# Optimization experiments

Hardware: AMD Instinct MI355X
Metric: run time of the kernel (lower is better)

The kernel has to match this reference:

```python
import jax, jax.numpy as jnp
import numpy as np

# Hardware-emulation constants (from init_kwargs, NeuroSim-style QLinear)
WL_IN = 8        # input activation bit width (bit-serial)
WL_W = 8         # weight bit width
CELL_BIT = 2     # bits per memory cell -> 4 weight slices
SUB = 128        # crossbar sub-array size (rows summed in analog)
ADC_BITS = 5     # ADC precision per partial sum
ONOFF = 10.0     # cell on/off conductance ratio
VARI = 0.05      # multiplicative device variation sigma


def _adc_quant(x, bits, axes):
    # LinearQuantizeOut: uniform quantization between tensor min/max
    mn = jnp.min(x, axis=axes, keepdims=True)
    mx = jnp.max(x, axis=axes, keepdims=True)
    step = (mx - mn) * (2.0 ** (-bits))
    step = jnp.where(step <= 0, 1.0, step)
    idx = jnp.clip(jnp.floor((x - mn) / step), 0.0, 2.0 ** bits - 1.0)
    return idx * step + mn


def _qlinear_hw(x, w, noise):
    """Analog PIM crossbar emulation of y = x @ w.T with bit-serial inputs,
    bit-sliced cells, on/off-ratio offset + dummy column, device variation,
    per-subarray ADC quantization."""
    B, N = x.shape
    F = w.shape[0]
    I, W, K = WL_IN, WL_W, WL_W // CELL_BIT
    cr = 2.0 ** CELL_BIT
    lower, upper = 1.0 / ONOFF, 1.0
    S = (N + SUB - 1) // SUB
    Np = S * SUB
    # quantize input to I bits in [0,1]; weight to W-bit integer in [0, 2^W-1]
    xq = jnp.round(jnp.clip(x, 0.0, 1.0) * (2.0 ** I - 1.0))            # [B, N]
    Xi = jnp.clip(jnp.round((w + 1.0) * 0.5 * (2.0 ** W - 1.0)), 0.0, 2.0 ** W - 1.0)  # [F, N]
    xq = jnp.pad(xq, ((0, 0), (0, Np - N)))
    Xi = jnp.pad(Xi, ((0, 0), (0, Np - N)))
    zpow = 2.0 ** jnp.arange(I, dtype=x.dtype)
    kpow = cr ** jnp.arange(K, dtype=x.dtype)
    bits = jnp.mod(jnp.floor(xq[..., None] / zpow), 2.0)                # [B, Np, I]
    slc = jnp.mod(jnp.floor(Xi[..., None] / kpow), cr)                  # [F, Np, K]
    g = slc * (upper - lower) + (cr - 1.0) * lower                      # cell conductances
    g = g * (1.0 + VARI * noise)                                        # device variation
    bits = bits.reshape(B, S, SUB, I)
    g = g.reshape(F, S, SUB, K)
    # analog partial sums per (input bit i, subarray s, weight slice k)
    P = jnp.einsum('bsai,fsak->iskbf', bits, g)                         # [I,S,K,B,F]
    # dummy column (all cells at lowest conductance), identical across F
    D = jnp.transpose(bits.sum(axis=2), (2, 1, 0)) * ((cr - 1.0) * lower)  # [I,S,B]
    Pq = _adc_quant(P, ADC_BITS, axes=(3, 4))
    Dq = _adc_quant(D, ADC_BITS, axes=(2,))
    scal = (2.0 ** jnp.arange(I, dtype=x.dtype))[:, None] * (cr ** jnp.arange(K, dtype=x.dtype))[None, :]
    acc = jnp.einsum('iskbf,ik->bf', Pq - Dq[:, :, None, :, None], scal) / (upper - lower)
    # undo integer mappings: w = 2*Xi/(2^W-1) - 1, x = xq/(2^I-1)
    out = 2.0 * acc / ((2.0 ** I - 1.0) * (2.0 ** W - 1.0)) \
          - xq.sum(axis=1, keepdims=True) / (2.0 ** I - 1.0)
    return out


def _qlinear(x, w, noise):
    # straight-through quantized weight (WAGE-style STE) + hardware forward
    Xi = jnp.clip(jnp.round((w + 1.0) * 0.5 * (2.0 ** WL_W - 1.0)), 0.0, 2.0 ** WL_W - 1.0)
    wq = 2.0 * Xi / (2.0 ** WL_W - 1.0) - 1.0
    wq_ste = w + jax.lax.stop_gradient(wq - w)
    out_ideal = x @ wq_ste.T
    out_hw = _qlinear_hw(x, w, noise)
    return out_ideal + jax.lax.stop_gradient(out_hw - out_ideal)


def setup_inputs() -> dict:
    key = jax.random.key(0)
    k1, k2, k3, k4, k5 = jax.random.split(key, 5)
    x = jax.random.uniform(k1, (1024, 784), dtype=jnp.float32)
    w1 = jax.random.normal(k2, (512, 784), dtype=jnp.float32) * 0.05
    w3 = jax.random.normal(k3, (10, 512), dtype=jnp.float32) * 0.08
    noise1 = jax.random.normal(k4, (512, 896, 4), dtype=jnp.float32)  # 784 padded to 7*128
    noise3 = jax.random.normal(k5, (10, 512, 4), dtype=jnp.float32)   # 512 = 4*128 exact
    return {"x": x, "w1": w1, "w3": w3, "noise1": noise1, "noise3": noise3}


def reference(x, w1, w3, noise1, noise3):
    h = jnp.tanh(_qlinear(x, w1, noise1))   # QLinear(784,512) + Tanh
    return _qlinear(h, w3, noise3)          # QLinear(512,10)
```

## Files before the change

### kernel.cpp

```cpp
#include <hip/hip_runtime.h>

#define FLTMAX 3.402823466e+38f


__device__ __forceinline__ void grid_barrier(unsigned* bar, int s, unsigned nblk)
{
    __syncthreads();
    if (threadIdx.x == 0) {
        unsigned* ctr = bar + s * 128;
        unsigned* rel = bar + 896 + s * 16;
        asm volatile("s_waitcnt vmcnt(0)" ::: "memory");
        __hip_atomic_fetch_add(&ctr[(blockIdx.x & 7) << 4], 1u,
                               __ATOMIC_RELAXED, __HIP_MEMORY_SCOPE_AGENT);
        if (blockIdx.x == 0) {
            for (int it = 0; it < (1 << 20); ++it) {
                unsigned tot = 0;
#pragma unroll
                for (int j = 0; j < 8; ++j)
                    tot += __hip_atomic_load(&ctr[j << 4], __ATOMIC_RELAXED,
                                             __HIP_MEMORY_SCOPE_AGENT);
                if (tot >= nblk) break;
                __builtin_amdgcn_s_sleep(8);
            }
            __hip_atomic_store(rel, 1u, __ATOMIC_RELAXED, __HIP_MEMORY_SCOPE_AGENT);
        } else {
            for (int it = 0; it < (1 << 20); ++it) {
                if (__hip_atomic_load(rel, __ATOMIC_RELAXED,
                                      __HIP_MEMORY_SCOPE_AGENT) != 0u)
                    break;
                __builtin_amdgcn_s_sleep(16);
            }
        }
    }
    __syncthreads();
}

__global__ void prep1_kernel(const float* __restrict__ x, float* __restrict__ sx1,
                             unsigned* __restrict__ xqbT, unsigned* __restrict__ stats1,
                             unsigned* __restrict__ bar)
{
    __shared__ float xr[896];
    __shared__ float red[128];
    int b = blockIdx.x;
    if (b == 0) {
        for (int t = threadIdx.x; t < 224; t += 128) {
            stats1[t * 2] = 0x7F7FFFFFu; stats1[t * 2 + 1] = 0u;
        }
        for (int t = threadIdx.x; t < 1008; t += 128) bar[t] = 0u;
    }
    float psum = 0.f;
    for (int n = threadIdx.x; n < 896; n += 128) {
        float v = 0.f;
        if (n < 784) {
            float xv = x[b * 784 + n];
            xv = fminf(fmaxf(xv, 0.f), 1.f);
            v = rintf(__fmul_rn(xv, 255.f));
        }
        xr[n] = v;
        psum += v;
    }
    red[threadIdx.x] = psum;
    __syncthreads();
    for (int w = 64; w >= 1; w >>= 1) {
        if (threadIdx.x < w) red[threadIdx.x] += red[threadIdx.x + w];
        __syncthreads();
    }
    if (threadIdx.x == 0) sx1[b] = red[0];
    if (threadIdx.x < 28) {
        int w = threadIdx.x;
        unsigned words[8] = {0, 0, 0, 0, 0, 0, 0, 0};
#pragma unroll 8
        for (int n = 0; n < 32; ++n) {
            int v = (int)xr[w * 32 + n];
#pragma unroll
            for (int i = 0; i < 8; ++i) words[i] |= ((unsigned)((v >> i) & 1)) << n;
        }
#pragma unroll
        for (int i = 0; i < 8; ++i) xqbT[(i * 28 + w) * 1024 + b] = words[i];
    }
}

__global__ void prepg1t_kernel(const float* __restrict__ w1, const float* __restrict__ noise1,
                               float* __restrict__ g1t)
{
    __shared__ float t[4][32][33];
    const int n0 = blockIdx.x * 32, f0 = blockIdx.y * 32;
    const int tid = threadIdx.x;
    {
        int n = tid & 31, fi = tid >> 5;
#pragma unroll
        for (int p = 0; p < 4; ++p) {
            int f = p * 8 + fi;
            int gn = n0 + n, gf = f0 + f;
            float gv[4] = {0.f, 0.f, 0.f, 0.f};
            if (gn < 784) {
                float w = w1[gf * 784 + gn];
                float Xi = fminf(fmaxf(rintf(__fmul_rn(__fmul_rn(__fadd_rn(w, 1.f), 0.5f), 255.f)),
                                       0.f), 255.f);
                int xi = (int)Xi;
                float4 nz = *(const float4*)&noise1[(gf * 896 + gn) * 4];
                float nzv[4] = {nz.x, nz.y, nz.z, nz.w};
#pragma unroll
                for (int k = 0; k < 4; ++k) {
                    int slc = (xi >> (2 * k)) & 3;
                    float base = __fadd_rn(__fmul_rn((float)slc, 0.9f), 0.3f);
                    float nf = __fadd_rn(1.f, __fmul_rn(0.05f, nzv[k]));
                    gv[k] = __fmul_rn(base, nf);
                }
            }
#pragma unroll
            for (int k = 0; k < 4; ++k) t[k][n][f] = gv[k];
        }
    }
    __syncthreads();
    {
        int f = tid & 31, nn = tid >> 5;
#pragma unroll
        for (int p = 0; p < 4; ++p) {
            int n = p * 8 + nn;
#pragma unroll
            for (int k = 0; k < 4; ++k)
                g1t[(n0 + n) * 2048 + k * 512 + f0 + f] = t[k][n][f];
        }
    }
}

__global__ void prepg2_kernel(const float* __restrict__ w3, const float* __restrict__ noise3,
                              float* __restrict__ g2t)
{
    int gid = blockIdx.x * 256 + threadIdx.x;
    if (gid >= 10 * 512) return;
    int f = gid / 512, n = gid % 512;
    float w = w3[f * 512 + n];
    float Xi = fminf(fmaxf(rintf(__fmul_rn(__fmul_rn(__fadd_rn(w, 1.f), 0.5f), 255.f)),
                           0.f), 255.f);
    int xi = (int)Xi;
#pragma unroll
    for (int k = 0; k < 4; ++k) {
        int slc = (xi >> (2 * k)) & 3;
        float base = __fadd_rn(__fmul_rn((float)slc, 0.9f), 0.3f);
        float nf = __fadd_rn(1.f, __fmul_rn(0.05f, noise3[(f * 512 + n) * 4 + k]));
        g2t[n * 40 + k * 10 + f] = __fmul_rn(base, nf);
    }
}

__global__ void dqpopT_kernel(const unsigned* __restrict__ xqbT, float* __restrict__ Dq)
{
    __shared__ float red[512];
    const int i = blockIdx.x / 7, s = blockIdx.x % 7;
    const int tid = threadIdx.x;
    float D[4];
    float mn = FLTMAX, mx = -FLTMAX;
#pragma unroll
    for (int u = 0; u < 4; ++u) {
        int b = tid + u * 256;
        int c = 0;
#pragma unroll
        for (int w = 0; w < 4; ++w)
            c += __popc(xqbT[(i * 28 + s * 4 + w) * 1024 + b]);
        D[u] = __fmul_rn((float)c, 0.3f);
        mn = fminf(mn, D[u]);
        mx = fmaxf(mx, D[u]);
    }
    red[tid] = mn; red[256 + tid] = mx;
    __syncthreads();
    for (int w = 128; w >= 1; w >>= 1) {
        if (tid < w) {
            red[tid] = fminf(red[tid], red[tid + w]);
            red[256 + tid] = fmaxf(red[256 + tid], red[256 + tid + w]);
        }
        __syncthreads();
    }
    mn = red[0]; mx = red[256];
    float step = __fmul_rn(__fsub_rn(mx, mn), 0.03125f);
    if (step <= 0.f) step = 1.f;
#pragma unroll
    for (int u = 0; u < 4; ++u) {
        int b = tid + u * 256;
        float idx = fminf(fmaxf(floorf(__fdiv_rn(__fsub_rn(D[u], mn), step)), 0.f), 31.f);
        Dq[(i * 7 + s) * 1024 + b] = __fadd_rn(__fmul_rn(idx, step), mn);
    }
}

__global__ void dqpop_kernel(const unsigned* __restrict__ xqb, float* __restrict__ Dq,
                             int S, int wpr)
{
    __shared__ float red[512];
    const int i = blockIdx.x / S, s = blockIdx.x % S;
    const int tid = threadIdx.x;
    float D[4];
    float mn = FLTMAX, mx = -FLTMAX;
#pragma unroll
    for (int u = 0; u < 4; ++u) {
        int b = tid + u * 256;
        uint4 w = *(const uint4*)&xqb[(i * 1024 + b) * wpr + s * 4];
        int c = __popc(w.x) + __popc(w.y) + __popc(w.z) + __popc(w.w);
        D[u] = __fmul_rn((float)c, 0.3f);
        mn = fminf(mn, D[u]);
        mx = fmaxf(mx, D[u]);
    }
    red[tid] = mn; red[256 + tid] = mx;
    __syncthreads();
    for (int w = 128; w >= 1; w >>= 1) {
        if (tid < w) {
            red[tid] = fminf(red[tid], red[tid + w]);
            red[256 + tid] = fmaxf(red[256 + tid], red[256 + tid + w]);
        }
        __syncthreads();
    }
    mn = red[0]; mx = red[256];
    float step = __fmul_rn(__fsub_rn(mx, mn), 0.03125f);
    if (step <= 0.f) step = 1.f;
#pragma unroll
    for (int u = 0; u < 4; ++u) {
        int b = tid + u * 256;
        float idx = fminf(fmaxf(floorf(__fdiv_rn(__fsub_rn(D[u], mn), step)), 0.f), 31.f);
        Dq[(i * S + s) * 1024 + b] = __fadd_rn(__fmul_rn(idx, step), mn);
    }
}

#define BK 32
__global__ __launch_bounds__(256, 2) void mm1_kernel(
    const unsigned* __restrict__ xqbT, const float* __restrict__ g1t,
    unsigned char* __restrict__ Pidx, unsigned* stats, unsigned* bar)
{
    __shared__ __align__(16) float Bs[BK][132];
    __shared__ unsigned Abits[256];
    __shared__ float red[512];
    __shared__ __align__(16) unsigned stage[2][128 * 33];
    const int tid = threadIdx.x;
    const int pair = blockIdx.x & 31;
    const int i = pair >> 2;
    const int bp = (pair & 3) * 256;
    const int btile0 = (pair * 2) & 7;
    const int colgrp = blockIdx.x >> 5;
    const int colBase = colgrp * 128;
    const int tx = tid & 15, ty = tid >> 4;
    const int aB = tid >> 5;
    const int eB = (tid & 31) << 2;
    const int k = colgrp >> 2;
    const int wv = tid >> 6, ln = tid & 63;
    const int rsub = ln >> 3, chunk = ln & 7;

    for (int s = 0; s < 7; ++s) {
        float4 pB[4];
#pragma unroll
        for (int u = 0; u < 4; ++u)
            pB[u] = *(const float4*)&g1t[(s * 128 + u * 8 + aB) * 2048 + colBase + eB];
        unsigned pAw = xqbT[(i * 28 + s * 4) * 1024 + bp + tid];

        float acc[2][8][8] = {};

        for (int ac = 0; ac < 4; ++ac) {
            __syncthreads();
#pragma unroll
            for (int u = 0; u < 4; ++u)
                *(float4*)&Bs[u * 8 + aB][eB] = pB[u];
            Abits[tid] = pAw;
            __syncthreads();

            if (ac < 3) {
                const int n0 = s * 128 + (ac + 1) * BK;
#pragma unroll
                for (int u = 0; u < 4; ++u)
                    pB[u] = *(const float4*)&g1t[(n0 + u * 8 + aB) * 2048 + colBase + eB];
                pAw = xqbT[(i * 28 + s * 4 + ac + 1) * 1024 + bp + tid];
            }

            unsigned wrd[2][8];
#pragma unroll
            for (int q = 0; q < 2; ++q)
#pragma unroll
                for (int u = 0; u < 4; ++u) {
                    wrd[q][u]     = Abits[q * 128 + (ty << 2) + u];
                    wrd[q][4 + u] = Abits[q * 128 + 64 + (ty << 2) + u];
                }

#pragma unroll 4
            for (int a = 0; a < BK; ++a) {
                float br[8];
                *(float4*)&br[0] = *(const float4*)&Bs[a][(tx << 2)];
                *(float4*)&br[4] = *(const float4*)&Bs[a][64 + (tx << 2)];
#pragma unroll
                for (int q = 0; q < 2; ++q)
#pragma unroll
                    for (int u = 0; u < 8; ++u) {
                        float ab = (float)((wrd[q][u] >> a) & 1u);
#pragma unroll
                        for (int v = 0; v < 8; ++v)
                            acc[q][u][v] = fmaf(ab, br[v], acc[q][u][v]);
                    }
            }
        }

        float mn = acc[0][0][0], mx = acc[0][0][0];
#pragma unroll
        for (int q = 0; q < 2; ++q)
#pragma unroll
            for (int u = 0; u < 8; ++u)
#pragma unroll
                for (int v = 0; v < 8; ++v) {
                    mn = fminf(mn, acc[q][u][v]); mx = fmaxf(mx, acc[q][u][v]);
                }
        red[tid] = mn; red[256 + tid] = mx;
        __syncthreads();
        for (int w = 128; w >= 1; w >>= 1) {
            if (tid < w) {
                red[tid] = fminf(red[tid], red[tid + w]);
                red[256 + tid] = fmaxf(red[256 + tid], red[256 + tid + w]);
            }
            __syncthreads();
        }
        const int slot = ((s * 8 + i) * 4 + k) * 2;
        if (tid == 0) {
            atomicMin(&stats[slot], __float_as_uint(red[0]));
            atomicMax(&stats[slot + 1], __float_as_uint(red[256]));
        }

        grid_barrier(bar, s, 512u);

        unsigned mnu = __hip_atomic_load(&stats[slot],     __ATOMIC_RELAXED,
                                         __HIP_MEMORY_SCOPE_AGENT);
        unsigned mxu = __hip_atomic_load(&stats[slot + 1], __ATOMIC_RELAXED,
                                         __HIP_MEMORY_SCOPE_AGENT);
        float qmn = __uint_as_float(mnu);
        float qmx = __uint_as_float(mxu);
        float step = __fmul_rn(__fsub_rn(qmx, qmn), 0.03125f);
        if (step <= 0.f) step = 1.f;

#pragma unroll
        for (int q = 0; q < 2; ++q)
#pragma unroll
            for (int uh = 0; uh < 2; ++uh)
#pragma unroll
                for (int u = 0; u < 4; ++u) {
                    int rr = uh * 64 + (ty << 2) + u;
#pragma unroll
                    for (int vh = 0; vh < 2; ++vh) {
                        float ix;
                        unsigned pack;
                        ix = fminf(fmaxf(floorf(__fdiv_rn(__fsub_rn(acc[q][uh * 4 + u][vh * 4 + 0], qmn), step)), 0.f), 31.f);
                        pack = (unsigned)(int)ix;
                        ix = fminf(fmaxf(floorf(__fdiv_rn(__fsub_rn(acc[q][uh * 4 + u][vh * 4 + 1], qmn), step)), 0.f), 31.f);
                        pack |= (unsigned)(int)ix << 8;
                        ix = fminf(fmaxf(floorf(__fdiv_rn(__fsub_rn(acc[q][uh * 4 + u][vh * 4 + 2], qmn), step)), 0.f), 31.f);
                        pack |= (unsigned)(int)ix << 16;
                        ix = fminf(fmaxf(floorf(__fdiv_rn(__fsub_rn(acc[q][uh * 4 + u][vh * 4 + 3], qmn), step)), 0.f), 31.f);
                        pack |= (unsigned)(int)ix << 24;
                        stage[q][rr * 33 + vh * 16 + tx] = pack;
                    }
                }
        __syncthreads();

#pragma unroll
        for (int q = 0; q < 2; ++q) {
            unsigned char* tbase = Pidx +
                ((size_t)(((s * 8 + i) * 16 + colgrp) * 8 + btile0 + q)) * 16384;
#pragma unroll
            for (int t = 0; t < 4; ++t) {
                int rr = t * 32 + wv * 8 + rsub;
                const unsigned* sp = &stage[q][rr * 33 + chunk * 4];
                uint4 v = make_uint4(sp[0], sp[1], sp[2], sp[3]);
                *(uint4*)&tbase[rr * 128 + chunk * 16] = v;
            }
        }
    }
}

__global__ void fold1_kernel(const unsigned char* __restrict__ Pidx,
                             const unsigned* __restrict__ stats,
                             const float* __restrict__ Dq1, const float* __restrict__ sx1,
                             float* __restrict__ xq2, unsigned* __restrict__ xqb2,
                             float* __restrict__ sx2)
{
    __shared__ float red[512];
    __shared__ float dt;
    __shared__ float2 st[224];
    int b = blockIdx.x;
    int f = threadIdx.x;
    if (f < 224) {
        float mn = __uint_as_float(stats[f * 2]);
        float mx = __uint_as_float(stats[f * 2 + 1]);
        float step = __fmul_rn(__fsub_rn(mx, mn), 0.03125f);
        if (step <= 0.f) step = 1.f;
        st[f] = make_float2(mn, step);
    }
    if (f == 0) {
        float sd = 0.f;
        for (int i = 0; i < 8; ++i) {
            float sc = (float)(85 << i);
            for (int ss = 0; ss < 7; ++ss) sd = fmaf(Dq1[(i * 7 + ss) * 1024 + b], sc, sd);
        }
        dt = sd;
    }
    __syncthreads();
    const int fhi = f >> 7, fl = f & 127;
    const unsigned char* pb = Pidx + (size_t)(b >> 7) * 16384
                                   + (size_t)(b & 127) * 128 + fl;
    float accR = 0.f;
    for (int s = 0; s < 7; ++s) {
        float sum = 0.f;
        for (int i = 0; i < 8; ++i) {
            const int si16 = (s * 8 + i) * 16;
#pragma unroll
            for (int kk = 0; kk < 4; ++kk) {
                float2 ms = st[((s * 8 + i) << 2) + kk];
                float ixv = (float)pb[(size_t)(si16 + kk * 4 + fhi) * 131072];
                float pq = __fadd_rn(__fmul_rn(ixv, ms.y), ms.x);
                sum = fmaf(pq, (float)(1 << (i + 2 * kk)), sum);
            }
        }
        accR = __fadd_rn(accR, sum);
    }
    float total = __fsub_rn(accR, dt);
    float acc = __fdiv_rn(total, 0.9f);
    float o = __fsub_rn(__fdiv_rn(__fmul_rn(2.f, acc), 65025.f), __fdiv_rn(sx1[b], 255.f));
    float h = tanhf(o);
    h = fminf(fmaxf(h, 0.f), 1.f);
    float code = rintf(__fmul_rn(h, 255.f));
    xq2[b * 512 + f] = code;
    int ci = (int)code;
    int lane = f & 63;
#pragma unroll
    for (int i = 0; i < 8; ++i) {
        unsigned long long m = __ballot((ci >> i) & 1);
        if ((lane & 31) == 0) {
            unsigned wv = (lane & 32) ? (unsigned)(m >> 32) : (unsigned)m;
            xqb2[(i * 1024 + b) * 16 + (f >> 5)] = wv;
        }
    }
    red[f] = code;
    __syncthreads();
    for (int w = 256; w >= 1; w >>= 1) {
        if (f < w) red[f] += red[f + w];
        __syncthreads();
    }
    if (f == 0) sx2[b] = red[0];
}

__global__ void mm2_kernel(const float* __restrict__ xq2, const float* __restrict__ g2t,
                           float* __restrict__ P2)
{
    int gid = blockIdx.x * 256 + threadIdx.x;
    if (gid >= 40960) return;
    int f = gid % 10;
    int b = (gid / 10) & 1023;
    int s = gid / 10240;
    float acc[8][4] = {};
    for (int a = 0; a < 128; ++a) {
        int n = s * 128 + a;
        int xi = (int)xq2[b * 512 + n];
        float g0 = g2t[n * 40 + f];
        float gA = g2t[n * 40 + 10 + f];
        float gB = g2t[n * 40 + 20 + f];
        float gC = g2t[n * 40 + 30 + f];
#pragma unroll
        for (int i = 0; i < 8; ++i) {
            float bi = (float)((xi >> i) & 1);
            acc[i][0] = fmaf(bi, g0, acc[i][0]);
            acc[i][1] = fmaf(bi, gA, acc[i][1]);
            acc[i][2] = fmaf(bi, gB, acc[i][2]);
            acc[i][3] = fmaf(bi, gC, acc[i][3]);
        }
    }
#pragma unroll
    for (int i = 0; i < 8; ++i)
#pragma unroll
        for (int k = 0; k < 4; ++k)
            P2[(size_t)((s * 8 + i) * 4 + k) * 10240 + b * 10 + f] = acc[i][k];
}

__global__ void stat2_kernel(const float* __restrict__ P2, float2* __restrict__ stats2)
{
    __shared__ float red[512];
    int p = blockIdx.x;
    int tid = threadIdx.x;
    float mn = FLTMAX, mx = -FLTMAX;
    for (int t = tid; t < 10240; t += 256) {
        float v = P2[(size_t)p * 10240 + t];
        mn = fminf(mn, v); mx = fmaxf(mx, v);
    }
    red[tid] = mn; red[256 + tid] = mx;
    __syncthreads();
    for (int w = 128; w >= 1; w >>= 1) {
        if (tid < w) {
            red[tid] = fminf(red[tid], red[tid + w]);
            red[256 + tid] = fmaxf(red[256 + tid], red[256 + tid + w]);
        }
        __syncthreads();
    }
    if (tid == 0) {
        float step = __fmul_rn(__fsub_rn(red[256], red[0]), 0.03125f);
        if (step <= 0.f) step = 1.f;
        stats2[p] = make_float2(red[0], step);
    }
}

__global__ void out2_kernel(const float* __restrict__ P2, const float2* __restrict__ stats2,
                            const float* __restrict__ Dq2, const float* __restrict__ sx2,
                            float* __restrict__ out)
{
    int gid = blockIdx.x * 256 + threadIdx.x;
    if (gid >= 10240) return;
    int b = gid / 10;
    float dt = 0.f;
    for (int i = 0; i < 8; ++i) {
        float sc = (float)(85 << i);
        for (int s = 0; s < 4; ++s) dt = fmaf(Dq2[(i * 4 + s) * 1024 + b], sc, dt);
    }
    float sum = 0.f;
    for (int s = 0; s < 4; ++s)
        for (int i = 0; i < 8; ++i)
#pragma unroll
            for (int k = 0; k < 4; ++k) {
                int p = (s * 8 + i) * 4 + k;
                float2 st = stats2[p];
                float val = P2[(size_t)p * 10240 + gid];
                float idx = fminf(fmaxf(floorf(__fdiv_rn(__fsub_rn(val, st.x), st.y)), 0.f), 31.f);
                float pq = __fadd_rn(__fmul_rn(idx, st.y), st.x);
                sum = fmaf(pq, (float)(1 << (i + 2 * k)), sum);
            }
    float total = __fsub_rn(sum, dt);
    float acc = __fdiv_rn(total, 0.9f);
    out[gid] = __fsub_rn(__fdiv_rn(__fmul_rn(2.f, acc), 65025.f), __fdiv_rn(sx2[b], 255.f));
}

extern "C" void kernel_launch(void* const* d_in, const int* in_sizes, int n_in,
                              void* d_out, int out_size, void* d_ws, size_t ws_size,
                              hipStream_t stream)
{
    const float* x      = (const float*)d_in[0];
    const float* w1     = (const float*)d_in[1];
    const float* w3     = (const float*)d_in[2];
    const float* noise1 = (const float*)d_in[3];
    const float* noise3 = (const float*)d_in[4];
    float* out = (float*)d_out;
    float* ws  = (float*)d_ws;

    float*         g1t    = ws + 0;
    float*         xq2    = ws + 1835008;
    float*         P2     = ws + 2359296;
    float*         g2t    = ws + 3670016;
    float*         Dq1    = ws + 3690496;
    float*         Dq2    = ws + 3747840;
    float*         sx1    = ws + 3780608;
    float*         sx2    = ws + 3781632;
    float2*        stats2 = (float2*)(ws + 3782656);
    unsigned*      stats1 = (unsigned*)(ws + 3782912);
    unsigned*      xqbT   = (unsigned*)(ws + 3783424);
    unsigned*      xqb2   = (unsigned*)(ws + 4012800);
    unsigned char* Pidx   = (unsigned char*)(ws + 4143872);
    unsigned*      bar    = (unsigned*)(ws + 33504256);

    prep1_kernel<<<1024, 128, 0, stream>>>(x, sx1, xqbT, stats1, bar);
    prepg1t_kernel<<<dim3(28, 16), 256, 0, stream>>>(w1, noise1, g1t);
    dqpopT_kernel<<<56, 256, 0, stream>>>(xqbT, Dq1);

    mm1_kernel<<<512, 256, 0, stream>>>(xqbT, g1t, Pidx, stats1, bar);

    fold1_kernel<<<1024, 512, 0, stream>>>(Pidx, stats1, Dq1, sx1, xq2, xqb2, sx2);
    prepg2_kernel<<<20, 256, 0, stream>>>(w3, noise3, g2t);
    dqpop_kernel<<<32, 256, 0, stream>>>(xqb2, Dq2, 4, 16);
    mm2_kernel<<<160, 256, 0, stream>>>(xq2, g2t, P2);
    stat2_kernel<<<128, 256, 0, stream>>>(P2, stats2);
    out2_kernel<<<40, 256, 0, stream>>>(P2, stats2, Dq2, sx2, out);
}
```

Baseline: 634.2 us.

## Replace grid-wide barrier with per-slot barriers and use packed FMA

Each persistent block used to wait at a grid-wide barrier after every subarray step. It now waits only on a per-statistics-slot counter that the 16 blocks sharing that ADC min/max slot increment, which removes global serialization across all 512 blocks. The inner accumulation is also rewritten with 2-wide float vectors so the compiler can emit packed FMA (v_pk_fma_f32) instructions. A trailing __syncthreads is added to protect the staging buffer, and the barrier memory cleared at startup grows to fit the per-slot counters.

```diff
diff --git a/kernel.cpp b/kernel.cpp
--- a/kernel.cpp
+++ b/kernel.cpp
@@ -2,34 +2,19 @@
 
 #define FLTMAX 3.402823466e+38f
 
-
-__device__ __forceinline__ void grid_barrier(unsigned* bar, int s, unsigned nblk)
+typedef float f32x2 __attribute__((ext_vector_type(2)));
+
+
+__device__ __forceinline__ void slot_barrier(unsigned* ctr, unsigned target)
 {
     __syncthreads();
     if (threadIdx.x == 0) {
-        unsigned* ctr = bar + s * 128;
-        unsigned* rel = bar + 896 + s * 16;
         asm volatile("s_waitcnt vmcnt(0)" ::: "memory");
-        __hip_atomic_fetch_add(&ctr[(blockIdx.x & 7) << 4], 1u,
-                               __ATOMIC_RELAXED, __HIP_MEMORY_SCOPE_AGENT);
-        if (blockIdx.x == 0) {
-            for (int it = 0; it < (1 << 20); ++it) {
-                unsigned tot = 0;
-#pragma unroll
-                for (int j = 0; j < 8; ++j)
-                    tot += __hip_atomic_load(&ctr[j << 4], __ATOMIC_RELAXED,
-                                             __HIP_MEMORY_SCOPE_AGENT);
-                if (tot >= nblk) break;
-                __builtin_amdgcn_s_sleep(8);
-            }
-            __hip_atomic_store(rel, 1u, __ATOMIC_RELAXED, __HIP_MEMORY_SCOPE_AGENT);
-        } else {
-            for (int it = 0; it < (1 << 20); ++it) {
-                if (__hip_atomic_load(rel, __ATOMIC_RELAXED,
-                                      __HIP_MEMORY_SCOPE_AGENT) != 0u)
-                    break;
-                __builtin_amdgcn_s_sleep(16);
-            }
+        __hip_atomic_fetch_add(ctr, 1u, __ATOMIC_RELAXED, __HIP_MEMORY_SCOPE_AGENT);
+        for (int it = 0; it < (1 << 22); ++it) {
+            if (__hip_atomic_load(ctr, __ATOMIC_RELAXED, __HIP_MEMORY_SCOPE_AGENT) >= target)
+                break;
+            __builtin_amdgcn_s_sleep(2);
         }
     }
     __syncthreads();
@@ -46,7 +31,7 @@
         for (int t = threadIdx.x; t < 224; t += 128) {
             stats1[t * 2] = 0x7F7FFFFFu; stats1[t * 2 + 1] = 0u;
         }
-        for (int t = threadIdx.x; t < 1008; t += 128) bar[t] = 0u;
+        for (int t = threadIdx.x; t < 3584; t += 128) bar[t] = 0u;
     }
     float psum = 0.f;
     for (int n = threadIdx.x; n < 896; n += 128) {
@@ -249,7 +234,7 @@
             pB[u] = *(const float4*)&g1t[(s * 128 + u * 8 + aB) * 2048 + colBase + eB];
         unsigned pAw = xqbT[(i * 28 + s * 4) * 1024 + bp + tid];
 
-        float acc[2][8][8] = {};
+        f32x2 acc[2][8][4] = {};
 
         for (int ac = 0; ac < 4; ++ac) {
             __syncthreads();
@@ -278,29 +263,33 @@
 
 #pragma unroll 4
             for (int a = 0; a < BK; ++a) {
-                float br[8];
-                *(float4*)&br[0] = *(const float4*)&Bs[a][(tx << 2)];
-                *(float4*)&br[4] = *(const float4*)&Bs[a][64 + (tx << 2)];
+                float4 b0 = *(const float4*)&Bs[a][(tx << 2)];
+                float4 b1 = *(const float4*)&Bs[a][64 + (tx << 2)];
+                f32x2 br[4];
+                br[0] = (f32x2){b0.x, b0.y}; br[1] = (f32x2){b0.z, b0.w};
+                br[2] = (f32x2){b1.x, b1.y}; br[3] = (f32x2){b1.z, b1.w};
 #pragma unroll
                 for (int q = 0; q < 2; ++q)
 #pragma unroll
                     for (int u = 0; u < 8; ++u) {
                         float ab = (float)((wrd[q][u] >> a) & 1u);
-#pragma unroll
-                        for (int v = 0; v < 8; ++v)
-                            acc[q][u][v] = fmaf(ab, br[v], acc[q][u][v]);
+                        f32x2 abv = {ab, ab};
+#pragma unroll
+                        for (int p = 0; p < 4; ++p)
+                            acc[q][u][p] = __builtin_elementwise_fma(abv, br[p], acc[q][u][p]);
                     }
             }
         }
 
-        float mn = acc[0][0][0], mx = acc[0][0][0];
+        float mn = acc[0][0][0].x, mx = acc[0][0][0].x;
 #pragma unroll
         for (int q = 0; q < 2; ++q)
 #pragma unroll
             for (int u = 0; u < 8; ++u)
 #pragma unroll
-                for (int v = 0; v < 8; ++v) {
-                    mn = fminf(mn, acc[q][u][v]); mx = fmaxf(mx, acc[q][u][v]);
+                for (int p = 0; p < 4; ++p) {
+                    mn = fminf(mn, acc[q][u][p].x); mx = fmaxf(mx, acc[q][u][p].x);
+                    mn = fminf(mn, acc[q][u][p].y); mx = fmaxf(mx, acc[q][u][p].y);
                 }
         red[tid] = mn; red[256 + tid] = mx;
         __syncthreads();
@@ -311,17 +300,17 @@
             }
             __syncthreads();
         }
-        const int slot = ((s * 8 + i) * 4 + k) * 2;
+        const int slot = ((s * 8 + i) * 4 + k);
         if (tid == 0) {
-            atomicMin(&stats[slot], __float_as_uint(red[0]));
-            atomicMax(&stats[slot + 1], __float_as_uint(red[256]));
-        }
-
-        grid_barrier(bar, s, 512u);
-
-        unsigned mnu = __hip_atomic_load(&stats[slot],     __ATOMIC_RELAXED,
+            atomicMin(&stats[slot * 2],     __float_as_uint(red[0]));
+            atomicMax(&stats[slot * 2 + 1], __float_as_uint(red[256]));
+        }
+
+        slot_barrier(&bar[slot * 16], 16u);
+
+        unsigned mnu = __hip_atomic_load(&stats[slot * 2],     __ATOMIC_RELAXED,
                                          __HIP_MEMORY_SCOPE_AGENT);
-        unsigned mxu = __hip_atomic_load(&stats[slot + 1], __ATOMIC_RELAXED,
+        unsigned mxu = __hip_atomic_load(&stats[slot * 2 + 1], __ATOMIC_RELAXED,
                                          __HIP_MEMORY_SCOPE_AGENT);
         float qmn = __uint_as_float(mnu);
         float qmx = __uint_as_float(mxu);
@@ -337,15 +326,17 @@
                     int rr = uh * 64 + (ty << 2) + u;
 #pragma unroll
                     for (int vh = 0; vh < 2; ++vh) {
+                        f32x2 e0 = acc[q][uh * 4 + u][vh * 2];
+                        f32x2 e1 = acc[q][uh * 4 + u][vh * 2 + 1];
                         float ix;
                         unsigned pack;
-                        ix = fminf(fmaxf(floorf(__fdiv_rn(__fsub_rn(acc[q][uh * 4 + u][vh * 4 + 0], qmn), step)), 0.f), 31.f);
+                        ix = fminf(fmaxf(floorf(__fdiv_rn(__fsub_rn(e0.x, qmn), step)), 0.f), 31.f);
                         pack = (unsigned)(int)ix;
-                        ix = fminf(fmaxf(floorf(__fdiv_rn(__fsub_rn(acc[q][uh * 4 + u][vh * 4 + 1], qmn), step)), 0.f), 31.f);
+                        ix = fminf(fmaxf(floorf(__fdiv_rn(__fsub_rn(e0.y, qmn), step)), 0.f), 31.f);
                         pack |= (unsigned)(int)ix << 8;
-                        ix = fminf(fmaxf(floorf(__fdiv_rn(__fsub_rn(acc[q][uh * 4 + u][vh * 4 + 2], qmn), step)), 0.f), 31.f);
+                        ix = fminf(fmaxf(floorf(__fdiv_rn(__fsub_rn(e1.x, qmn), step)), 0.f), 31.f);
                         pack |= (unsigned)(int)ix << 16;
-                        ix = fminf(fmaxf(floorf(__fdiv_rn(__fsub_rn(acc[q][uh * 4 + u][vh * 4 + 3], qmn), step)), 0.f), 31.f);
+                        ix = fminf(fmaxf(floorf(__fdiv_rn(__fsub_rn(e1.y, qmn), step)), 0.f), 31.f);
                         pack |= (unsigned)(int)ix << 24;
                         stage[q][rr * 33 + vh * 16 + tx] = pack;
                     }
@@ -364,6 +355,7 @@
                 *(uint4*)&tbase[rr * 128 + chunk * 16] = v;
             }
         }
+        __syncthreads();
     }
 }
 
```

After: 624.6 us. Within noise of the previous version (-1.5%).
